# Performance work log

Hardware: AMD Instinct MI355X
Metric: run time of the kernel (lower is better)

## Reference

```python
import jax, jax.numpy as jnp
import numpy as np

MODEL_DIM = 1024
NUM_HEADS = 8
B, L = 16, 2048


def setup_inputs() -> dict:
    key = jax.random.key(0)
    ks = jax.random.split(key, 12)
    s = 1.0 / np.sqrt(MODEL_DIM)
    d = MODEL_DIM
    return {
        "query": jax.random.normal(ks[0], (B, L, d), jnp.float32),
        "key_": jax.random.normal(ks[1], (B, L, d), jnp.float32),
        "value": jax.random.normal(ks[2], (B, L, d), jnp.float32),
        "Wq": jax.random.uniform(ks[3], (d, d), jnp.float32, -s, s),
        "bq": jax.random.uniform(ks[4], (d,), jnp.float32, -s, s),
        "Wk": jax.random.uniform(ks[5], (d, d), jnp.float32, -s, s),
        "bk": jax.random.uniform(ks[6], (d,), jnp.float32, -s, s),
        "Wv": jax.random.uniform(ks[7], (d, d), jnp.float32, -s, s),
        "bv": jax.random.uniform(ks[8], (d,), jnp.float32, -s, s),
        "Wo": jax.random.uniform(ks[9], (d, d), jnp.float32, -s, s),
        "bo": jax.random.uniform(ks[10], (d,), jnp.float32, -s, s),
    }


def reference(query, key_, value, Wq, bq, Wk, bk, Wv, bv, Wo, bo):
    # NOTE: the original module does NOT split heads; attention is over the
    # full model_dim per batch row. num_heads only enters via the scale.
    residual = query
    q = jnp.einsum("bld,de->ble", query, Wq) + bq
    k = jnp.einsum("bld,de->ble", key_, Wk) + bk
    v = jnp.einsum("bld,de->ble", value, Wv) + bv
    scale = (MODEL_DIM // NUM_HEADS) ** (-0.5)
    attn = jnp.einsum("bqd,bkd->bqk", q, k) * scale  # [B, L, L]
    attn = jax.nn.softmax(attn, axis=-1)
    ctx = jnp.einsum("bqk,bkd->bqd", attn, v)
    out = jnp.einsum("bld,de->ble", ctx, Wo) + bo  # dropout=0.0 -> identity
    return residual + out
```

## Files before the change

kernel.cpp:

```cpp
#include <hip/hip_runtime.h>
#include <cstdint>

#define B_ 16
#define L_ 2048
#define D_ 1024
#define BLROWS (B_ * L_)
#define QK_SCALE 0.08838834764831845f

typedef unsigned short u16;
typedef __attribute__((ext_vector_type(8))) __bf16 bf16x8;
typedef __attribute__((ext_vector_type(4))) float f32x4;
typedef __attribute__((ext_vector_type(4))) unsigned int u32x4;
typedef __attribute__((ext_vector_type(4))) u16 u16x4;

__device__ __forceinline__ u16 f2bf(float f) {
  unsigned u = __builtin_bit_cast(unsigned, f);
  u += 0x7fffu + ((u >> 16) & 1u);
  return (u16)(u >> 16);
}
__device__ __forceinline__ float bf2f(unsigned hu) {
  return __builtin_bit_cast(float, hu << 16);
}

__device__ __forceinline__ void gll16(const void* g, void* l) {
  auto gp = reinterpret_cast<const __attribute__((address_space(1))) unsigned int*>(
      reinterpret_cast<uintptr_t>(g));
  auto lp = reinterpret_cast<__attribute__((address_space(3))) unsigned int*>(
      reinterpret_cast<uintptr_t>(l));
  __builtin_amdgcn_global_load_lds(gp, lp, 16, 0, 0);
}

typedef __attribute__((ext_vector_type(4))) float fv4;
__global__ void convert_bf16(const fv4* __restrict__ in, u16x4* __restrict__ out, int n4) {
  int i = blockIdx.x * blockDim.x + threadIdx.x;
  const int stride = gridDim.x * blockDim.x;
  for (; i < n4; i += stride) {
    fv4 v = in[i];
    u16x4 o;
    o.x = f2bf(v.x); o.y = f2bf(v.y); o.z = f2bf(v.z); o.w = f2bf(v.w);
    out[i] = o;
  }
}

__global__ void transpose_convert_1k(const float* __restrict__ W, u16* __restrict__ WT) {
  __shared__ float tile[32][33];
  const int bx = blockIdx.x * 32;
  const int by = blockIdx.y * 32;
  const int tx = threadIdx.x & 31;
  const int ty = threadIdx.x >> 5;
#pragma unroll
  for (int j = 0; j < 4; ++j) {
    const int r = ty + j * 8;
    tile[r][tx] = W[(size_t)(by + r) * 1024 + bx + tx];
  }
  __syncthreads();
#pragma unroll
  for (int j = 0; j < 4; ++j) {
    const int r = ty + j * 8;
    WT[(size_t)(bx + r) * 1024 + by + tx] = f2bf(tile[tx][r]);
  }
}

__global__ void softmax_rows(u16* __restrict__ S) {
  const size_t row = blockIdx.x;
  u32x4* p = (u32x4*)(S + row * 2048);
  const int t = threadIdx.x;
  u32x4 v = p[t];
  unsigned vv[4] = {v.x, v.y, v.z, v.w};
  float x[8];
#pragma unroll
  for (int i = 0; i < 4; ++i) {
    x[2 * i]     = bf2f(vv[i] & 0xffffu);
    x[2 * i + 1] = bf2f(vv[i] >> 16);
  }
  float m = x[0];
#pragma unroll
  for (int i = 1; i < 8; ++i) m = fmaxf(m, x[i]);
#pragma unroll
  for (int off = 32; off > 0; off >>= 1) m = fmaxf(m, __shfl_xor(m, off));
  __shared__ float red[4];
  const int w = t >> 6, l = t & 63;
  if (l == 0) red[w] = m;
  __syncthreads();
  m = fmaxf(fmaxf(red[0], red[1]), fmaxf(red[2], red[3]));
  float e[8], s = 0.f;
#pragma unroll
  for (int i = 0; i < 8; ++i) { e[i] = __expf(x[i] - m); s += e[i]; }
#pragma unroll
  for (int off = 32; off > 0; off >>= 1) s += __shfl_xor(s, off);
  __syncthreads();
  if (l == 0) red[w] = s;
  __syncthreads();
  s = red[0] + red[1] + red[2] + red[3];
  const float inv = 1.0f / s;
  unsigned oo[4];
#pragma unroll
  for (int i = 0; i < 4; ++i) {
    oo[i] = (unsigned)f2bf(e[2 * i] * inv) | ((unsigned)f2bf(e[2 * i + 1] * inv) << 16);
  }
  u32x4 o; o.x = oo[0]; o.y = oo[1]; o.z = oo[2]; o.w = oo[3];
  p[t] = o;
}


template <int OUT_BF16, int BIAS_MODE, int RESID>
__global__ __launch_bounds__(512) void gemm8(
    const u16* __restrict__ A, const u16* __restrict__ Bm, void* __restrict__ Cv,
    const float* __restrict__ bias, const float* __restrict__ resid,
    int N, int K, float scale, long long sA, long long sB, long long sC,
    int gm, int gn) {
  __shared__ alignas(16) u16 lds[4][16384];

  const int nwg = gridDim.x;
  const int wg = blockIdx.x;
  const int q = nwg >> 3, rr = nwg & 7;
  const int xcd = wg & 7, idx = wg >> 3;
  const int wgid = (xcd < rr ? xcd * (q + 1) : rr * (q + 1) + (xcd - rr) * q) + idx;
  const int z = wgid / (gm * gn);
  const int rem = wgid - z * gm * gn;
  const int my = rem / gn;
  const int nx = rem - my * gn;
  const int m0 = my * 256, n0 = nx * 256;

  A  += (long long)z * sA;
  Bm += (long long)z * sB;

  const int t = threadIdx.x;
  const int w = t >> 6;
  const int l = t & 63;
  const int wm = w >> 2;
  const int wn = w & 3;
  const int lr = l & 15;
  const int lk = l >> 4;

  const int s8  = (t & 7) ^ ((t >> 3) & 7);
  const int rst = 2 * (t >> 3) + (s8 >> 2);
  const int kst = (s8 & 3) * 8;
  const u16* pA0 = A  + (long long)(m0 + rst) * K + kst;
  const u16* pA1 = A  + (long long)(m0 + 128 + rst) * K + kst;
  const u16* pB0 = Bm + (long long)(n0 + rst) * K + kst;
  const u16* pB1 = Bm + (long long)(n0 + 128 + rst) * K + kst;
  const int wbase = w * 512;

#define STAGEU(U, BUFP)                              \
  gll16(pA0 + (U) * 32, (BUFP) + wbase);             \
  gll16(pA1 + (U) * 32, (BUFP) + 4096 + wbase);      \
  gll16(pB0 + (U) * 32, (BUFP) + 8192 + wbase);      \
  gll16(pB1 + (U) * 32, (BUFP) + 12288 + wbase);

  const int lh = lr >> 1;
  const int swz = ((((lr & 1) * 4 + lk) ^ lh) * 8);
  const int axo = (wm * 64 + lh) * 64 + swz;
  const int bxo = 8192 + (wn * 32 + lh) * 64 + swz;

  f32x4 acc[8][4];
#pragma unroll
  for (int i = 0; i < 8; ++i)
#pragma unroll
    for (int j = 0; j < 4; ++j) acc[i][j] = f32x4{0.f, 0.f, 0.f, 0.f};

  u16* Lb = &lds[0][0];

  STAGEU(0, Lb)
  STAGEU(1, Lb + 16384)
  STAGEU(2, Lb + 32768)
  asm volatile("s_waitcnt vmcnt(8)" ::: "memory");
  __builtin_amdgcn_s_barrier();
  __builtin_amdgcn_sched_barrier(0);

  const int NT = K >> 5;
  for (int u = 0; u < NT; ++u) {
    const u16* cb = Lb + (u & 3) * 16384;
    u16* sb = Lb + ((u + 3) & 3) * 16384;

    bf16x8 af[4], bf[4], ag[4];

    if (u + 3 < NT) { STAGEU(u + 3, sb) }
#pragma unroll
    for (int mf = 0; mf < 4; ++mf)
      af[mf] = __builtin_bit_cast(bf16x8, *(const u32x4*)&cb[axo + mf * 512]);
#pragma unroll
    for (int nf = 0; nf < 4; ++nf)
      bf[nf] = __builtin_bit_cast(bf16x8, *(const u32x4*)&cb[bxo + nf * 512]);
    __builtin_amdgcn_s_barrier();
    __builtin_amdgcn_s_setprio(1);
#pragma unroll
    for (int mf = 0; mf < 4; ++mf)
#pragma unroll
      for (int nf = 0; nf < 4; ++nf)
        acc[mf][nf] =
            __builtin_amdgcn_mfma_f32_16x16x32_bf16(af[mf], bf[nf], acc[mf][nf], 0, 0, 0);
    __builtin_amdgcn_s_setprio(0);
    __builtin_amdgcn_s_barrier();

#pragma unroll
    for (int mf = 0; mf < 4; ++mf)
      ag[mf] = __builtin_bit_cast(bf16x8, *(const u32x4*)&cb[axo + (mf + 4) * 512]);
    __builtin_amdgcn_s_barrier();
    __builtin_amdgcn_s_setprio(1);
#pragma unroll
    for (int mf = 0; mf < 4; ++mf)
#pragma unroll
      for (int nf = 0; nf < 4; ++nf)
        acc[mf + 4][nf] =
            __builtin_amdgcn_mfma_f32_16x16x32_bf16(ag[mf], bf[nf], acc[mf + 4][nf], 0, 0, 0);
    __builtin_amdgcn_s_setprio(0);

    if (u + 3 < NT)      { asm volatile("s_waitcnt vmcnt(8)" ::: "memory"); }
    else if (u + 2 < NT) { asm volatile("s_waitcnt vmcnt(4)" ::: "memory"); }
    else if (u + 1 < NT) { asm volatile("s_waitcnt vmcnt(0)" ::: "memory"); }
    __builtin_amdgcn_s_barrier();
    __builtin_amdgcn_sched_barrier(0);
  }

  const int crow0 = m0 + wm * 128;
  const int ccol0 = n0 + wn * 64;
#pragma unroll
  for (int mi = 0; mi < 8; ++mi) {
#pragma unroll
    for (int i = 0; i < 4; ++i) {
      const int grow = crow0 + mi * 16 + lk * 4 + i;
#pragma unroll
      for (int nj = 0; nj < 4; ++nj) {
        const int gcol = ccol0 + nj * 16 + lr;
        float v = acc[mi][nj][i] * scale;
        if (BIAS_MODE == 1) v += bias[gcol];
        if (BIAS_MODE == 2) v += bias[grow];
        if (RESID) v += resid[(long long)grow * N + gcol];
        const long long cidx = (long long)z * sC + (long long)grow * N + gcol;
        if (OUT_BF16) ((u16*)Cv)[cidx] = f2bf(v);
        else          ((float*)Cv)[cidx] = v;
      }
    }
  }
}

extern "C" void kernel_launch(void* const* d_in, const int* in_sizes, int n_in,
                              void* d_out, int out_size, void* d_ws, size_t ws_size,
                              hipStream_t stream) {
  const float* query = (const float*)d_in[0];
  const float* key_  = (const float*)d_in[1];
  const float* value = (const float*)d_in[2];
  const float* Wq = (const float*)d_in[3];
  const float* bq = (const float*)d_in[4];
  const float* Wk = (const float*)d_in[5];
  const float* bk = (const float*)d_in[6];
  const float* Wv = (const float*)d_in[7];
  const float* bv = (const float*)d_in[8];
  const float* Wo = (const float*)d_in[9];
  const float* bo = (const float*)d_in[10];
  float* out = (float*)d_out;

  char* ws = (char*)d_ws;
  u16* xq  = (u16*)(ws + 0);
  u16* xk  = (u16*)(ws + 67108864);
  u16* xv  = (u16*)(ws + 134217728);
  u16* wqt = (u16*)(ws + 201326592);
  u16* wkt = (u16*)(ws + 203423744);
  u16* wvt = (u16*)(ws + 205520896);
  u16* wot = (u16*)(ws + 207618048);
  u16* qb  = (u16*)(ws + 209715200);
  u16* kb  = (u16*)(ws + 276824064);
  u16* vt  = (u16*)(ws + 343932928);
  u16* sp  = (u16*)(ws + 0);
  u16* ctx = (u16*)(ws + 134217728);

  const dim3 blk(256);
  const dim3 blk8(512);
  const int n4 = BLROWS * D_ / 4;

  convert_bf16<<<2048, blk, 0, stream>>>((const fv4*)query, (u16x4*)xq, n4);
  convert_bf16<<<2048, blk, 0, stream>>>((const fv4*)key_,  (u16x4*)xk, n4);
  convert_bf16<<<2048, blk, 0, stream>>>((const fv4*)value, (u16x4*)xv, n4);
  transpose_convert_1k<<<dim3(32, 32), blk, 0, stream>>>(Wq, wqt);
  transpose_convert_1k<<<dim3(32, 32), blk, 0, stream>>>(Wk, wkt);
  transpose_convert_1k<<<dim3(32, 32), blk, 0, stream>>>(Wv, wvt);
  transpose_convert_1k<<<dim3(32, 32), blk, 0, stream>>>(Wo, wot);

  gemm8<1, 1, 0><<<dim3(512), blk8, 0, stream>>>(
      xq, wqt, qb, bq, nullptr, D_, D_, 1.0f, 0, 0, 0, 128, 4);
  gemm8<1, 1, 0><<<dim3(512), blk8, 0, stream>>>(
      xk, wkt, kb, bk, nullptr, D_, D_, 1.0f, 0, 0, 0, 128, 4);
  gemm8<1, 2, 0><<<dim3(512), blk8, 0, stream>>>(
      wvt, xv, vt, bv, nullptr, L_, D_, 1.0f,
      0, (long long)L_ * D_, (long long)D_ * L_, 4, 8);
  gemm8<1, 0, 0><<<dim3(1024), blk8, 0, stream>>>(
      qb, kb, sp, nullptr, nullptr, L_, D_, QK_SCALE,
      (long long)L_ * D_, (long long)L_ * D_, (long long)L_ * L_, 8, 8);
  softmax_rows<<<BLROWS, blk, 0, stream>>>(sp);
  gemm8<1, 0, 0><<<dim3(512), blk8, 0, stream>>>(
      sp, vt, ctx, nullptr, nullptr, D_, L_, 1.0f,
      (long long)L_ * L_, (long long)D_ * L_, (long long)L_ * D_, 8, 4);
  gemm8<0, 1, 1><<<dim3(512), blk8, 0, stream>>>(
      ctx, wot, out, bo, query, D_, D_, 1.0f, 0, 0, 0, 128, 4);

  (void)in_sizes; (void)n_in; (void)out_size; (void)ws_size;
}
```

Baseline: 1.129 ms.

## Switch GEMM to BK=64 double-buffered pipeline with quadrant-split MFMA phases

Replaces the 4-stage BK=32 LDS ring with a 2-stage BK=64 double buffer and a new XOR swizzle. Each k-tile's MFMA work is split into four quadrant phases, and the next A and B tiles are issued into the just-consumed buffer partway through the iteration. This halves the loop trip count and the per-iteration barrier overhead, at the cost of a shallower prefetch depth and more live fragment registers.

```diff
diff --git a/kernel.cpp b/kernel.cpp
--- a/kernel.cpp
+++ b/kernel.cpp
@@ -109,7 +109,7 @@
     const float* __restrict__ bias, const float* __restrict__ resid,
     int N, int K, float scale, long long sA, long long sB, long long sC,
     int gm, int gn) {
-  __shared__ alignas(16) u16 lds[4][16384];
+  __shared__ alignas(16) u16 lds[2][32768];
 
   const int nwg = gridDim.x;
   const int wg = blockIdx.x;
@@ -133,25 +133,29 @@
   const int lr = l & 15;
   const int lk = l >> 4;
 
-  const int s8  = (t & 7) ^ ((t >> 3) & 7);
-  const int rst = 2 * (t >> 3) + (s8 >> 2);
-  const int kst = (s8 & 3) * 8;
-  const u16* pA0 = A  + (long long)(m0 + rst) * K + kst;
-  const u16* pA1 = A  + (long long)(m0 + 128 + rst) * K + kst;
-  const u16* pB0 = Bm + (long long)(n0 + rst) * K + kst;
-  const u16* pB1 = Bm + (long long)(n0 + 128 + rst) * K + kst;
+  const int rl = t >> 3;
+  const int kc8 = ((t & 7) ^ (rl & 7)) * 8;
+  const u16* sa = A  + (long long)(m0 + rl) * K + kc8;
+  const u16* sb = Bm + (long long)(n0 + rl) * K + kc8;
+  const long long rK = 64LL * K;
   const int wbase = w * 512;
 
-#define STAGEU(U, BUFP)                              \
-  gll16(pA0 + (U) * 32, (BUFP) + wbase);             \
-  gll16(pA1 + (U) * 32, (BUFP) + 4096 + wbase);      \
-  gll16(pB0 + (U) * 32, (BUFP) + 8192 + wbase);      \
-  gll16(pB1 + (U) * 32, (BUFP) + 12288 + wbase);
-
-  const int lh = lr >> 1;
-  const int swz = ((((lr & 1) * 4 + lk) ^ lh) * 8);
-  const int axo = (wm * 64 + lh) * 64 + swz;
-  const int bxo = 8192 + (wn * 32 + lh) * 64 + swz;
+#define STAGE_A(TT, BUF)                                        \
+  gll16(sa + 0 * rK + (TT) * 64, (BUF) +     0 + wbase);        \
+  gll16(sa + 1 * rK + (TT) * 64, (BUF) +  4096 + wbase);        \
+  gll16(sa + 2 * rK + (TT) * 64, (BUF) +  8192 + wbase);        \
+  gll16(sa + 3 * rK + (TT) * 64, (BUF) + 12288 + wbase);
+#define STAGE_B(TT, BUF)                                        \
+  gll16(sb + 0 * rK + (TT) * 64, (BUF) + 16384 + wbase);        \
+  gll16(sb + 1 * rK + (TT) * 64, (BUF) + 20480 + wbase);        \
+  gll16(sb + 2 * rK + (TT) * 64, (BUF) + 24576 + wbase);        \
+  gll16(sb + 3 * rK + (TT) * 64, (BUF) + 28672 + wbase);
+
+  const int sw = lr & 7;
+  const int c0 = ((0 + lk) ^ sw) * 8;
+  const int c1 = ((4 + lk) ^ sw) * 8;
+  const int a0 = (wm * 128 + lr) * 64;
+  const int b0 = 16384 + (wn * 64 + lr) * 64;
 
   f32x4 acc[8][4];
 #pragma unroll
@@ -159,56 +163,95 @@
 #pragma unroll
     for (int j = 0; j < 4; ++j) acc[i][j] = f32x4{0.f, 0.f, 0.f, 0.f};
 
-  u16* Lb = &lds[0][0];
-
-  STAGEU(0, Lb)
-  STAGEU(1, Lb + 16384)
-  STAGEU(2, Lb + 32768)
+  STAGE_A(0, &lds[0][0])
+  STAGE_B(0, &lds[0][0])
+  STAGE_A(1, &lds[1][0])
+  STAGE_B(1, &lds[1][0])
   asm volatile("s_waitcnt vmcnt(8)" ::: "memory");
   __builtin_amdgcn_s_barrier();
   __builtin_amdgcn_sched_barrier(0);
 
-  const int NT = K >> 5;
+  const int NT = K >> 6;
   for (int u = 0; u < NT; ++u) {
-    const u16* cb = Lb + (u & 3) * 16384;
-    u16* sb = Lb + ((u + 3) & 3) * 16384;
-
-    bf16x8 af[4], bf[4], ag[4];
-
-    if (u + 3 < NT) { STAGEU(u + 3, sb) }
+    u16* cb = &lds[u & 1][0];
+    const bool pf = (u + 2 < NT);
+
+    bf16x8 af[4][2], ag[4][2], b0f[2][2], b1f[2][2];
+
+#pragma unroll
+    for (int mf = 0; mf < 4; ++mf) {
+      af[mf][0] = __builtin_bit_cast(bf16x8, *(const u32x4*)&cb[a0 + mf * 1024 + c0]);
+      af[mf][1] = __builtin_bit_cast(bf16x8, *(const u32x4*)&cb[a0 + mf * 1024 + c1]);
+    }
+#pragma unroll
+    for (int nf = 0; nf < 2; ++nf) {
+      b0f[nf][0] = __builtin_bit_cast(bf16x8, *(const u32x4*)&cb[b0 + nf * 1024 + c0]);
+      b0f[nf][1] = __builtin_bit_cast(bf16x8, *(const u32x4*)&cb[b0 + nf * 1024 + c1]);
+    }
+    __builtin_amdgcn_s_barrier();
+    __builtin_amdgcn_s_setprio(1);
 #pragma unroll
     for (int mf = 0; mf < 4; ++mf)
-      af[mf] = __builtin_bit_cast(bf16x8, *(const u32x4*)&cb[axo + mf * 512]);
-#pragma unroll
-    for (int nf = 0; nf < 4; ++nf)
-      bf[nf] = __builtin_bit_cast(bf16x8, *(const u32x4*)&cb[bxo + nf * 512]);
+#pragma unroll
+      for (int nf = 0; nf < 2; ++nf)
+#pragma unroll
+        for (int kk = 0; kk < 2; ++kk)
+          acc[mf][nf] = __builtin_amdgcn_mfma_f32_16x16x32_bf16(
+              af[mf][kk], b0f[nf][kk], acc[mf][nf], 0, 0, 0);
+    __builtin_amdgcn_s_setprio(0);
+    __builtin_amdgcn_s_barrier();
+
+#pragma unroll
+    for (int mf = 0; mf < 4; ++mf) {
+      ag[mf][0] = __builtin_bit_cast(bf16x8, *(const u32x4*)&cb[a0 + 4096 + mf * 1024 + c0]);
+      ag[mf][1] = __builtin_bit_cast(bf16x8, *(const u32x4*)&cb[a0 + 4096 + mf * 1024 + c1]);
+    }
     __builtin_amdgcn_s_barrier();
     __builtin_amdgcn_s_setprio(1);
 #pragma unroll
     for (int mf = 0; mf < 4; ++mf)
 #pragma unroll
-      for (int nf = 0; nf < 4; ++nf)
-        acc[mf][nf] =
-            __builtin_amdgcn_mfma_f32_16x16x32_bf16(af[mf], bf[nf], acc[mf][nf], 0, 0, 0);
+      for (int nf = 0; nf < 2; ++nf)
+#pragma unroll
+        for (int kk = 0; kk < 2; ++kk)
+          acc[mf + 4][nf] = __builtin_amdgcn_mfma_f32_16x16x32_bf16(
+              ag[mf][kk], b0f[nf][kk], acc[mf + 4][nf], 0, 0, 0);
     __builtin_amdgcn_s_setprio(0);
     __builtin_amdgcn_s_barrier();
 
+    if (pf) { STAGE_A(u + 2, cb) }
+#pragma unroll
+    for (int nf = 0; nf < 2; ++nf) {
+      b1f[nf][0] = __builtin_bit_cast(bf16x8, *(const u32x4*)&cb[b0 + 2048 + nf * 1024 + c0]);
+      b1f[nf][1] = __builtin_bit_cast(bf16x8, *(const u32x4*)&cb[b0 + 2048 + nf * 1024 + c1]);
+    }
+    __builtin_amdgcn_s_barrier();
+    __builtin_amdgcn_s_setprio(1);
 #pragma unroll
     for (int mf = 0; mf < 4; ++mf)
-      ag[mf] = __builtin_bit_cast(bf16x8, *(const u32x4*)&cb[axo + (mf + 4) * 512]);
-    __builtin_amdgcn_s_barrier();
+#pragma unroll
+      for (int nf = 0; nf < 2; ++nf)
+#pragma unroll
+        for (int kk = 0; kk < 2; ++kk)
+          acc[mf + 4][nf + 2] = __builtin_amdgcn_mfma_f32_16x16x32_bf16(
+              ag[mf][kk], b1f[nf][kk], acc[mf + 4][nf + 2], 0, 0, 0);
+    __builtin_amdgcn_s_setprio(0);
+    __builtin_amdgcn_s_barrier();
+
+    if (pf) { STAGE_B(u + 2, cb) }
     __builtin_amdgcn_s_setprio(1);
 #pragma unroll
     for (int mf = 0; mf < 4; ++mf)
 #pragma unroll
-      for (int nf = 0; nf < 4; ++nf)
-        acc[mf + 4][nf] =
-            __builtin_amdgcn_mfma_f32_16x16x32_bf16(ag[mf], bf[nf], acc[mf + 4][nf], 0, 0, 0);
+      for (int nf = 0; nf < 2; ++nf)
+#pragma unroll
+        for (int kk = 0; kk < 2; ++kk)
+          acc[mf][nf + 2] = __builtin_amdgcn_mfma_f32_16x16x32_bf16(
+              af[mf][kk], b1f[nf][kk], acc[mf][nf + 2], 0, 0, 0);
     __builtin_amdgcn_s_setprio(0);
 
-    if (u + 3 < NT)      { asm volatile("s_waitcnt vmcnt(8)" ::: "memory"); }
-    else if (u + 2 < NT) { asm volatile("s_waitcnt vmcnt(4)" ::: "memory"); }
-    else if (u + 1 < NT) { asm volatile("s_waitcnt vmcnt(0)" ::: "memory"); }
+    if (pf)                { asm volatile("s_waitcnt vmcnt(8)" ::: "memory"); }
+    else if (u + 1 < NT)   { asm volatile("s_waitcnt vmcnt(0)" ::: "memory"); }
     __builtin_amdgcn_s_barrier();
     __builtin_amdgcn_sched_barrier(0);
   }
```

Measured after the change: 1.065 ms. 5.7% less time.
